# Kernel optimization log

Measured on AMD Instinct MI355X. Metric: run time of the kernel, lower is better.

Reference implementation:

```python
import jax, jax.numpy as jnp
import numpy as np

B, N, DIM = 2, 2048, 1024
NUM_HEADS = 16
EFF = NUM_HEADS // 2          # 8 effective heads
HD = DIM // NUM_HEADS         # 64
LAMBDA_INIT = 0.8
EPS = 1e-5


def setup_inputs() -> dict:
    key = jax.random.key(0)
    ks = jax.random.split(key, 16)
    s = 0.02
    return {
        "x":  jax.random.normal(ks[0], (B, N, DIM), dtype=jnp.float32),
        "Wq": jax.random.normal(ks[1], (DIM, DIM), dtype=jnp.float32) * s,
        "bq": jnp.zeros((DIM,), dtype=jnp.float32),
        "Wk": jax.random.normal(ks[2], (DIM, DIM), dtype=jnp.float32) * s,
        "bk": jnp.zeros((DIM,), dtype=jnp.float32),
        "Wv": jax.random.normal(ks[3], (DIM, DIM), dtype=jnp.float32) * s,
        "bv": jnp.zeros((DIM,), dtype=jnp.float32),
        "Wo": jax.random.normal(ks[4], (DIM, DIM), dtype=jnp.float32) * s,
        "bo": jnp.zeros((DIM,), dtype=jnp.float32),
        "norm_w": jnp.ones((2 * HD,), dtype=jnp.float32),
        "lq1": jax.random.normal(ks[5], (HD,), dtype=jnp.float32) * 0.1,
        "lk1": jax.random.normal(ks[6], (HD,), dtype=jnp.float32) * 0.1,
        "lq2": jax.random.normal(ks[7], (HD,), dtype=jnp.float32) * 0.1,
        "lk2": jax.random.normal(ks[8], (HD,), dtype=jnp.float32) * 0.1,
    }


def reference(x, Wq, bq, Wk, bk, Wv, bv, Wo, bo, norm_w, lq1, lk1, lq2, lk2):
    scale = HD ** -0.5
    # projections (torch Linear: y = x @ W.T + b)
    q = (x @ Wq.T + bq).reshape(B, N, NUM_HEADS, HD).transpose(0, 2, 1, 3) * scale  # [B,2E,N,hd]
    k = (x @ Wk.T + bk).reshape(B, N, NUM_HEADS, HD).transpose(0, 2, 1, 3)          # [B,2E,N,hd]
    v = (x @ Wv.T + bv).reshape(B, N, EFF, 2 * HD).transpose(0, 2, 1, 3)            # [B,E,N,2hd]

    scores = jnp.einsum('bhqd,bhkd->bhqk', q, k)              # [B,2E,N,N]
    probs = jax.nn.softmax(scores, axis=-1)
    probs = probs.reshape(B, EFF, 2, N, N)                    # pair consecutive heads

    lam = jnp.exp(jnp.sum(lq1 * lk1)) - jnp.exp(jnp.sum(lq2 * lk2)) + LAMBDA_INIT
    diff = probs[:, :, 0] - lam * probs[:, :, 1]              # [B,E,N,N]

    out = jnp.einsum('behk,bekd->behd'.replace('e','h').replace('hh','h') if False else 'bhqk,bhkd->bhqd', diff, v)  # [B,E,N,2hd]
    # headwise RMSNorm over last dim (2*hd)
    out = out * jax.lax.rsqrt(jnp.mean(out * out, axis=-1, keepdims=True) + EPS) * norm_w
    out = out * (1.0 - LAMBDA_INIT)

    out = out.transpose(0, 2, 1, 3).reshape(B, N, DIM)
    return out @ Wo.T + bo
```

## Files before the change

kernel.cpp:

```cpp
#include <hip/hip_runtime.h>
#include <hip/hip_bf16.h>

#define B_   2
#define N_   2048
#define DIM_ 1024
#define HD_  64
#define DV_  128

typedef __bf16 bf16;
typedef __bf16 bf16x8 __attribute__((ext_vector_type(8)));
typedef __bf16 bf16x4 __attribute__((ext_vector_type(4)));
typedef float  floatx4 __attribute__((ext_vector_type(4)));
typedef float  floatx16 __attribute__((ext_vector_type(16)));
typedef unsigned int uint;
typedef uint uint2v __attribute__((ext_vector_type(2)));
typedef uint uint4v __attribute__((ext_vector_type(4)));

#if __has_builtin(__builtin_amdgcn_exp2f)
#define EXP2(x) __builtin_amdgcn_exp2f(x)
#else
#define EXP2(x) exp2f(x)
#endif

#define QSCALE 0.1803368801111244f

__device__ __forceinline__ void async16(const void* g, void* l) {
  __builtin_amdgcn_global_load_lds(
      (__attribute__((address_space(1))) void*)g,
      (__attribute__((address_space(3))) void*)l, 16, 0, 0);
}

__device__ __forceinline__ uint packbf(float a, float b) {
  unsigned short ul = __builtin_bit_cast(unsigned short, (bf16)a);
  unsigned short uh = __builtin_bit_cast(unsigned short, (bf16)b);
  return (uint)ul | ((uint)uh << 16);
}

__global__ void convert_kernel(const float* __restrict__ x,
                               const float* __restrict__ wq,
                               const float* __restrict__ wk,
                               const float* __restrict__ wv,
                               const float* __restrict__ wo,
                               bf16* __restrict__ dst) {
  const int NX = B_ * N_ * DIM_;
  const int NW = DIM_ * DIM_;
  int i = (blockIdx.x * 256 + threadIdx.x) * 4;
  const float* src;
  int off;
  if (i < NX) { src = x; off = i; }
  else {
    int j = i - NX;
    int w = j >> 20;
    off = j & (NW - 1);
    src = (w == 0) ? wq : (w == 1) ? wk : (w == 2) ? wv : wo;
  }
  float4 v = *(const float4*)(src + off);
  bf16x4 o = { (bf16)v.x, (bf16)v.y, (bf16)v.z, (bf16)v.w };
  *(bf16x4*)(dst + i) = o;
}

__global__ void lam_kernel(const float* __restrict__ lq1, const float* __restrict__ lk1,
                           const float* __restrict__ lq2, const float* __restrict__ lk2,
                           float* __restrict__ lam_out) {
  int l = threadIdx.x;
  float a = lq1[l] * lk1[l];
  float b = lq2[l] * lk2[l];
  for (int m = 1; m < 64; m <<= 1) {
    a += __shfl_xor(a, m, 64);
    b += __shfl_xor(b, m, 64);
  }
  if (l == 0) *lam_out = __expf(a) - __expf(b) + 0.8f;
}

__global__ __launch_bounds__(256) void proj_kernel(
    const bf16* __restrict__ xb, const bf16* __restrict__ wall,
    const float* __restrict__ bq, const float* __restrict__ bk,
    const float* __restrict__ bv,
    bf16* __restrict__ qo, bf16* __restrict__ ko, bf16* __restrict__ vt) {
  __shared__ __align__(16) bf16 SM[2 * 128 * 64];
  bf16* At = SM;
  bf16* Bt = SM + 128 * 64;
  const int tid = threadIdx.x, lane = tid & 63, w = tid >> 6;
  const int tm = blockIdx.x, tn = blockIdx.y, z = blockIdx.z;
  const int quad = lane >> 4, l15 = lane & 15;
  const int wm = (w >> 1) * 64, wn = (w & 1) * 64;
  const bf16* Ab = xb + (long)tm * 128 * DIM_;
  const bf16* Bb = wall + (long)z * (DIM_ * DIM_) + (long)tn * 128 * DIM_;
  floatx4 zero = {0.f, 0.f, 0.f, 0.f};
  floatx4 acc[4][4];
#pragma unroll
  for (int i = 0; i < 4; ++i)
#pragma unroll
    for (int j = 0; j < 4; ++j) acc[i][j] = zero;

  for (int kb = 0; kb < DIM_ / 64; ++kb) {
    for (int idx = tid; idx < 1024; idx += 256) {
      int row = idx >> 3, ch = idx & 7, g = ch ^ (row & 7);
      async16(Ab + row * DIM_ + kb * 64 + g * 8, (char*)At + (idx - lane) * 16);
      async16(Bb + row * DIM_ + kb * 64 + g * 8, (char*)Bt + (idx - lane) * 16);
    }
    __syncthreads();
#pragma unroll
    for (int ks = 0; ks < 2; ++ks) {
      bf16x8 af[4], bfm[4];
#pragma unroll
      for (int mt = 0; mt < 4; ++mt) {
        int r = wm + mt * 16 + l15;
        af[mt] = *(const bf16x8*)&At[r * 64 + ((ks * 4 + quad) ^ (r & 7)) * 8];
      }
#pragma unroll
      for (int nt = 0; nt < 4; ++nt) {
        int r = wn + nt * 16 + l15;
        bfm[nt] = *(const bf16x8*)&Bt[r * 64 + ((ks * 4 + quad) ^ (r & 7)) * 8];
      }
#pragma unroll
      for (int mt = 0; mt < 4; ++mt)
#pragma unroll
        for (int nt = 0; nt < 4; ++nt)
          acc[mt][nt] = __builtin_amdgcn_mfma_f32_16x16x32_bf16(
              af[mt], bfm[nt], acc[mt][nt], 0, 0, 0);
    }
    __syncthreads();
  }

  if (z != 2) {
#pragma unroll
    for (int mt = 0; mt < 4; ++mt)
#pragma unroll
      for (int nt = 0; nt < 4; ++nt)
#pragma unroll
        for (int r = 0; r < 4; ++r) {
          int grow = tm * 128 + wm + mt * 16 + quad * 4 + r;
          int gcol = tn * 128 + wn + nt * 16 + l15;
          float v = acc[mt][nt][r];
          if (z == 0) {
            qo[(long)grow * DIM_ + gcol] = (bf16)((v + bq[gcol]) * QSCALE);
          } else {
            ko[(long)grow * DIM_ + gcol] = (bf16)(v + bk[gcol]);
          }
        }
  } else {
    bf16* Vl = SM;
#pragma unroll
    for (int nt = 0; nt < 4; ++nt) {
      int d = wn + nt * 16 + l15;
      float bvv = bv[tn * 128 + d];
      int m = (d & 7) * 2;
#pragma unroll
      for (int mt = 0; mt < 4; ++mt) {
        bf16x4 v4 = { (bf16)(acc[mt][nt][0] + bvv), (bf16)(acc[mt][nt][1] + bvv),
                      (bf16)(acc[mt][nt][2] + bvv), (bf16)(acc[mt][nt][3] + bvv) };
        int c = (wm >> 2) + mt * 4 + quad;
        *(bf16x4*)&Vl[d * 128 + (c ^ m) * 4] = v4;
      }
    }
    __syncthreads();
    const int bb = tm >> 4, e = tn;
    const long rowbase = ((long)(bb * 8 + e) * 128) * (long)N_ + (tm & 15) * 128;
#pragma unroll
    for (int p = 0; p < 8; ++p) {
      int d = p * 16 + (tid >> 4), j = tid & 15;
      int cs = (2 * j) ^ ((d & 7) * 2);
      bf16x8 val = *(const bf16x8*)&Vl[d * 128 + cs * 4];
      *(bf16x8*)&vt[rowbase + (long)d * N_ + j * 8] = val;
    }
  }
}

__global__ __launch_bounds__(256, 1) void attn_kernel(
    const bf16* __restrict__ qb, const bf16* __restrict__ kbuf,
    const bf16* __restrict__ vt, const float* __restrict__ lamp,
    const float* __restrict__ norm_w, bf16* __restrict__ ao) {
  __shared__ __align__(16) char smem[65536];

  const int tid = threadIdx.x, lane = tid & 63, w = tid >> 6;
  const int qt = blockIdx.x, e = blockIdx.y, b = blockIdx.z;
  const int hl = w & 1, qh = w >> 1;
  const int h = lane >> 5, l31 = lane & 31;
  const int qbase = qt * 128 + qh * 64;

  bf16x8 qf[2][4];
#pragma unroll
  for (int qs = 0; qs < 2; ++qs) {
    const bf16* qrp = qb + (long)(b * N_ + qbase + qs * 32 + l31) * DIM_
                      + e * 128 + hl * 64 + h * 8;
#pragma unroll
    for (int c = 0; c < 4; ++c) qf[qs][c] = *(const bf16x8*)(qrp + c * 16);
  }

  const bf16* kbase = kbuf + (long)b * N_ * DIM_ + e * 128;
  const bf16* vbase = vt + (long)(b * 8 + e) * DV_ * N_;

  floatx16 acc[2][4];
#pragma unroll
  for (int qs = 0; qs < 2; ++qs)
#pragma unroll
    for (int dt = 0; dt < 4; ++dt) acc[qs][dt] = floatx16{};
  float lp[2] = {0.f, 0.f};

#define STAGE(ktv, bufv)                                                            \
  {                                                                                 \
    int kt_ = (ktv);                                                                \
    char* kdst = smem + (bufv) * 16384;                                             \
    char* vdst = smem + 32768 + (bufv) * 16384;                                     \
    _Pragma("unroll") for (int t = 0; t < 4; ++t) {                                 \
      int idx = tid + t * 256;                                                      \
      int khl = idx >> 9, row = (idx >> 3) & 63, ch = idx & 7;                      \
      int g = ch ^ (row & 7) ^ ((row >> 3) & 3);                                    \
      async16(kbase + ((long)(kt_ * 64 + row)) * DIM_ + khl * 64 + g * 8,           \
              kdst + (idx - lane) * 16);                                            \
    }                                                                               \
    _Pragma("unroll") for (int t = 0; t < 4; ++t) {                                 \
      int idx = tid + t * 256;                                                      \
      int row = idx >> 3, ch = idx & 7;                                             \
      int g = ch ^ (row & 7) ^ ((row >> 3) & 3);                                    \
      async16(vbase + (long)row * N_ + kt_ * 64 + g * 8,                            \
              vdst + (idx - lane) * 16);                                            \
    }                                                                               \
  }

  STAGE(0, 0);

  for (int kt = 0; kt < N_ / 64; ++kt) {
    const int buf = kt & 1;
    __syncthreads();
    if (kt + 1 < N_ / 64) STAGE(kt + 1, buf ^ 1);

    const bf16* Kh = (const bf16*)(smem + buf * 16384) + hl * 4096;
    const bf16* Vb = (const bf16*)(smem + 32768 + buf * 16384);

    bf16x8 kfrag[2][4], vfrag[4][4];
#pragma unroll
    for (int kt2 = 0; kt2 < 2; ++kt2)
#pragma unroll
      for (int c = 0; c < 4; ++c) {
        int row = kt2 * 32 + l31;
        int sw = (c * 2 + h) ^ (row & 7) ^ ((row >> 3) & 3);
        kfrag[kt2][c] = *(const bf16x8*)&Kh[row * 64 + sw * 8];
      }
#pragma unroll
    for (int dt = 0; dt < 4; ++dt)
#pragma unroll
      for (int kc = 0; kc < 4; ++kc) {
        int row = dt * 32 + l31;
        int sw = (kc * 2 + h) ^ (row & 7) ^ ((row >> 3) & 3);
        vfrag[dt][kc] = *(const bf16x8*)&Vb[row * 64 + sw * 8];
      }

#pragma unroll
    for (int qs = 0; qs < 2; ++qs) {
      bf16x8 af[2][2];
#pragma unroll
      for (int kt2 = 0; kt2 < 2; ++kt2) {
        floatx16 sv{};
#pragma unroll
        for (int c = 0; c < 4; ++c)
          sv = __builtin_amdgcn_mfma_f32_32x32x16_bf16(kfrag[kt2][c], qf[qs][c], sv, 0, 0, 0);
        float t[16];
        float s = 0.f;
#pragma unroll
        for (int i = 0; i < 16; ++i) { t[i] = EXP2(sv[i]); s += t[i]; }
        lp[qs] += s;
        uint d0 = packbf(t[0], t[1]),   d1 = packbf(t[2], t[3]);
        uint d2 = packbf(t[4], t[5]),   d3 = packbf(t[6], t[7]);
        uint d4 = packbf(t[8], t[9]),   d5 = packbf(t[10], t[11]);
        uint d6 = packbf(t[12], t[13]), d7 = packbf(t[14], t[15]);
        uint4v f0, f1;
#if __has_builtin(__builtin_amdgcn_permlane32_swap)
        uint2v r02 = __builtin_amdgcn_permlane32_swap(d0, d2, false, false);
        uint2v r13 = __builtin_amdgcn_permlane32_swap(d1, d3, false, false);
        f0 = uint4v{r02.x, r13.x, r02.y, r13.y};
        uint2v r46 = __builtin_amdgcn_permlane32_swap(d4, d6, false, false);
        uint2v r57 = __builtin_amdgcn_permlane32_swap(d5, d7, false, false);
        f1 = uint4v{r46.x, r57.x, r46.y, r57.y};
#else
        uint e0 = __shfl_xor((int)d0, 32, 64), e1 = __shfl_xor((int)d1, 32, 64);
        uint e2 = __shfl_xor((int)d2, 32, 64), e3 = __shfl_xor((int)d3, 32, 64);
        uint e4 = __shfl_xor((int)d4, 32, 64), e5 = __shfl_xor((int)d5, 32, 64);
        uint e6 = __shfl_xor((int)d6, 32, 64), e7 = __shfl_xor((int)d7, 32, 64);
        f0 = h ? uint4v{e2, e3, d2, d3} : uint4v{d0, d1, e0, e1};
        f1 = h ? uint4v{e6, e7, d6, d7} : uint4v{d4, d5, e4, e5};
#endif
        af[kt2][0] = __builtin_bit_cast(bf16x8, f0);
        af[kt2][1] = __builtin_bit_cast(bf16x8, f1);
      }
#pragma unroll
      for (int dt = 0; dt < 4; ++dt)
#pragma unroll
        for (int kt2 = 0; kt2 < 2; ++kt2)
#pragma unroll
          for (int u = 0; u < 2; ++u)
            acc[qs][dt] = __builtin_amdgcn_mfma_f32_32x32x16_bf16(
                af[kt2][u], vfrag[dt][kt2 * 2 + u], acc[qs][dt], 0, 0, 0);
    }
  }

  lp[0] += __shfl_xor(lp[0], 32, 64);
  lp[1] += __shfl_xor(lp[1], 32, 64);

  float* Ob = (float*)smem;
  __syncthreads();

  if (hl == 1) {
#pragma unroll
    for (int qs = 0; qs < 2; ++qs)
#pragma unroll
      for (int r = 0; r < 16; ++r) {
        int qloc = (r & 3) + 8 * (r >> 2) + 4 * h;
        float inv = 1.0f / __shfl(lp[qs], qloc, 64);
        float* row = &Ob[(qh * 64 + qs * 32 + qloc) * 128 + l31];
#pragma unroll
        for (int dt = 0; dt < 4; ++dt) row[dt * 32] = acc[qs][dt][r] * inv;
      }
  }
  __syncthreads();
  if (hl == 0) {
    float lam = *lamp;
    float nw4[4];
#pragma unroll
    for (int dt = 0; dt < 4; ++dt) nw4[dt] = norm_w[dt * 32 + l31] * 0.2f;
#pragma unroll
    for (int qs = 0; qs < 2; ++qs)
#pragma unroll
      for (int r = 0; r < 16; ++r) {
        int qloc = (r & 3) + 8 * (r >> 2) + 4 * h;
        float inv = 1.0f / __shfl(lp[qs], qloc, 64);
        const float* row = &Ob[(qh * 64 + qs * 32 + qloc) * 128 + l31];
        float v[4], ss = 0.f;
#pragma unroll
        for (int dt = 0; dt < 4; ++dt) {
          v[dt] = acc[qs][dt][r] * inv - lam * row[dt * 32];
          ss += v[dt] * v[dt];
        }
#pragma unroll
        for (int msk = 1; msk < 32; msk <<= 1) ss += __shfl_xor(ss, msk, 64);
        float rms = rsqrtf(ss * (1.0f / 128.0f) + 1e-5f);
        int n = qbase + qs * 32 + qloc;
        bf16* dst = ao + (long)(b * N_ + n) * DIM_ + e * DV_ + l31;
#pragma unroll
        for (int dt = 0; dt < 4; ++dt) dst[dt * 32] = (bf16)(v[dt] * rms * nw4[dt]);
      }
  }
}

__global__ __launch_bounds__(512) void out_gemm(
    const bf16* __restrict__ ab, const bf16* __restrict__ wo,
    const float* __restrict__ bo, float* __restrict__ out) {
  __shared__ __align__(16) bf16 At[128 * 64];
  __shared__ __align__(16) bf16 Bt[128 * 64];
  const int tid = threadIdx.x, lane = tid & 63, w = tid >> 6;
  const int tm = blockIdx.x, tn = blockIdx.y;
  const int quad = lane >> 4, l15 = lane & 15;
  const int wm = (w & 3) * 32, wn = (w >> 2) * 64;
  const bf16* Ab = ab + (long)tm * 128 * DIM_;
  const bf16* Bb = wo + (long)tn * 128 * DIM_;
  floatx4 zero = {0.f, 0.f, 0.f, 0.f};
  floatx4 acc[2][4];
#pragma unroll
  for (int i = 0; i < 2; ++i)
#pragma unroll
    for (int j = 0; j < 4; ++j) acc[i][j] = zero;

  for (int kb = 0; kb < DIM_ / 64; ++kb) {
    for (int idx = tid; idx < 1024; idx += 512) {
      int row = idx >> 3, ch = idx & 7, g = ch ^ (row & 7);
      async16(Ab + row * DIM_ + kb * 64 + g * 8, (char*)At + (idx - lane) * 16);
      async16(Bb + row * DIM_ + kb * 64 + g * 8, (char*)Bt + (idx - lane) * 16);
    }
    __syncthreads();
#pragma unroll
    for (int ks = 0; ks < 2; ++ks) {
      bf16x8 af[2], bfm[4];
#pragma unroll
      for (int mt = 0; mt < 2; ++mt) {
        int r = wm + mt * 16 + l15;
        af[mt] = *(const bf16x8*)&At[r * 64 + ((ks * 4 + quad) ^ (r & 7)) * 8];
      }
#pragma unroll
      for (int nt = 0; nt < 4; ++nt) {
        int r = wn + nt * 16 + l15;
        bfm[nt] = *(const bf16x8*)&Bt[r * 64 + ((ks * 4 + quad) ^ (r & 7)) * 8];
      }
#pragma unroll
      for (int mt = 0; mt < 2; ++mt)
#pragma unroll
        for (int nt = 0; nt < 4; ++nt)
          acc[mt][nt] = __builtin_amdgcn_mfma_f32_16x16x32_bf16(
              af[mt], bfm[nt], acc[mt][nt], 0, 0, 0);
    }
    __syncthreads();
  }
#pragma unroll
  for (int mt = 0; mt < 2; ++mt)
#pragma unroll
    for (int nt = 0; nt < 4; ++nt)
#pragma unroll
      for (int r = 0; r < 4; ++r) {
        int grow = tm * 128 + wm + mt * 16 + quad * 4 + r;
        int gcol = tn * 128 + wn + nt * 16 + l15;
        out[(long)grow * DIM_ + gcol] = acc[mt][nt][r] + bo[gcol];
      }
}

extern "C" void kernel_launch(void* const* d_in, const int* in_sizes, int n_in,
                              void* d_out, int out_size, void* d_ws, size_t ws_size,
                              hipStream_t stream) {
  const float* x    = (const float*)d_in[0];
  const float* Wq   = (const float*)d_in[1];
  const float* bq   = (const float*)d_in[2];
  const float* Wk   = (const float*)d_in[3];
  const float* bk   = (const float*)d_in[4];
  const float* Wv   = (const float*)d_in[5];
  const float* bv   = (const float*)d_in[6];
  const float* Wo   = (const float*)d_in[7];
  const float* bo   = (const float*)d_in[8];
  const float* nw   = (const float*)d_in[9];
  const float* lq1  = (const float*)d_in[10];
  const float* lk1  = (const float*)d_in[11];
  const float* lq2  = (const float*)d_in[12];
  const float* lk2  = (const float*)d_in[13];

  char* ws = (char*)d_ws;
  float* lam = (float*)ws;
  bf16* xb   = (bf16*)(ws + 256);
  bf16* wqb  = xb + 4194304;
  bf16* qb   = wqb + 4 * 1048576;
  bf16* kbuf = qb + 4194304;
  bf16* vtb  = kbuf + 4194304;
  bf16* ab   = vtb + 4194304;

  convert_kernel<<<8192, 256, 0, stream>>>(x, Wq, Wk, Wv, Wo, xb);
  lam_kernel<<<1, 64, 0, stream>>>(lq1, lk1, lq2, lk2, lam);
  proj_kernel<<<dim3(32, 8, 3), 256, 0, stream>>>(xb, wqb, bq, bk, bv, qb, kbuf, vtb);
  attn_kernel<<<dim3(16, 8, 2), 256, 0, stream>>>(qb, kbuf, vtb, lam, nw, ab);
  out_gemm<<<dim3(32, 8), 512, 0, stream>>>(ab, wqb + 3 * 1048576, bo, (float*)d_out);
}
```

Before: 222.5 us.

## Split attention work across 8 waves with one 32-row query slice each

```diff
diff --git a/kernel.cpp b/kernel.cpp
--- a/kernel.cpp
+++ b/kernel.cpp
@@ -167,7 +167,7 @@
   }
 }
 
-__global__ __launch_bounds__(256, 1) void attn_kernel(
+__global__ __launch_bounds__(512, 2) void attn_kernel(
     const bf16* __restrict__ qb, const bf16* __restrict__ kbuf,
     const bf16* __restrict__ vt, const float* __restrict__ lamp,
     const float* __restrict__ norm_w, bf16* __restrict__ ao) {
@@ -177,41 +177,38 @@
   const int qt = blockIdx.x, e = blockIdx.y, b = blockIdx.z;
   const int hl = w & 1, qh = w >> 1;
   const int h = lane >> 5, l31 = lane & 31;
-  const int qbase = qt * 128 + qh * 64;
-
-  bf16x8 qf[2][4];
-#pragma unroll
-  for (int qs = 0; qs < 2; ++qs) {
-    const bf16* qrp = qb + (long)(b * N_ + qbase + qs * 32 + l31) * DIM_
+  const int qbase = qt * 128;
+
+  bf16x8 qf[4];
+  {
+    const bf16* qrp = qb + (long)(b * N_ + qbase + qh * 32 + l31) * DIM_
                       + e * 128 + hl * 64 + h * 8;
 #pragma unroll
-    for (int c = 0; c < 4; ++c) qf[qs][c] = *(const bf16x8*)(qrp + c * 16);
+    for (int c = 0; c < 4; ++c) qf[c] = *(const bf16x8*)(qrp + c * 16);
   }
 
   const bf16* kbase = kbuf + (long)b * N_ * DIM_ + e * 128;
   const bf16* vbase = vt + (long)(b * 8 + e) * DV_ * N_;
 
-  floatx16 acc[2][4];
-#pragma unroll
-  for (int qs = 0; qs < 2; ++qs)
-#pragma unroll
-    for (int dt = 0; dt < 4; ++dt) acc[qs][dt] = floatx16{};
-  float lp[2] = {0.f, 0.f};
+  floatx16 acc[4];
+#pragma unroll
+  for (int dt = 0; dt < 4; ++dt) acc[dt] = floatx16{};
+  float lp = 0.f;
 
 #define STAGE(ktv, bufv)                                                            \
   {                                                                                 \
     int kt_ = (ktv);                                                                \
     char* kdst = smem + (bufv) * 16384;                                             \
     char* vdst = smem + 32768 + (bufv) * 16384;                                     \
-    _Pragma("unroll") for (int t = 0; t < 4; ++t) {                                 \
-      int idx = tid + t * 256;                                                      \
+    _Pragma("unroll") for (int t = 0; t < 2; ++t) {                                 \
+      int idx = tid + t * 512;                                                      \
       int khl = idx >> 9, row = (idx >> 3) & 63, ch = idx & 7;                      \
       int g = ch ^ (row & 7) ^ ((row >> 3) & 3);                                    \
       async16(kbase + ((long)(kt_ * 64 + row)) * DIM_ + khl * 64 + g * 8,           \
               kdst + (idx - lane) * 16);                                            \
     }                                                                               \
-    _Pragma("unroll") for (int t = 0; t < 4; ++t) {                                 \
-      int idx = tid + t * 256;                                                      \
+    _Pragma("unroll") for (int t = 0; t < 2; ++t) {                                 \
+      int idx = tid + t * 512;                                                      \
       int row = idx >> 3, ch = idx & 7;                                             \
       int g = ch ^ (row & 7) ^ ((row >> 3) & 3);                                    \
       async16(vbase + (long)row * N_ + kt_ * 64 + g * 8,                            \
@@ -247,71 +244,65 @@
         vfrag[dt][kc] = *(const bf16x8*)&Vb[row * 64 + sw * 8];
       }
 
-#pragma unroll
-    for (int qs = 0; qs < 2; ++qs) {
-      bf16x8 af[2][2];
-#pragma unroll
-      for (int kt2 = 0; kt2 < 2; ++kt2) {
-        floatx16 sv{};
-#pragma unroll
-        for (int c = 0; c < 4; ++c)
-          sv = __builtin_amdgcn_mfma_f32_32x32x16_bf16(kfrag[kt2][c], qf[qs][c], sv, 0, 0, 0);
-        float t[16];
-        float s = 0.f;
-#pragma unroll
-        for (int i = 0; i < 16; ++i) { t[i] = EXP2(sv[i]); s += t[i]; }
-        lp[qs] += s;
-        uint d0 = packbf(t[0], t[1]),   d1 = packbf(t[2], t[3]);
-        uint d2 = packbf(t[4], t[5]),   d3 = packbf(t[6], t[7]);
-        uint d4 = packbf(t[8], t[9]),   d5 = packbf(t[10], t[11]);
-        uint d6 = packbf(t[12], t[13]), d7 = packbf(t[14], t[15]);
-        uint4v f0, f1;
+    bf16x8 af[2][2];
+#pragma unroll
+    for (int kt2 = 0; kt2 < 2; ++kt2) {
+      floatx16 sv{};
+#pragma unroll
+      for (int c = 0; c < 4; ++c)
+        sv = __builtin_amdgcn_mfma_f32_32x32x16_bf16(kfrag[kt2][c], qf[c], sv, 0, 0, 0);
+      float t[16];
+      float s = 0.f;
+#pragma unroll
+      for (int i = 0; i < 16; ++i) { t[i] = EXP2(sv[i]); s += t[i]; }
+      lp += s;
+      uint d0 = packbf(t[0], t[1]),   d1 = packbf(t[2], t[3]);
+      uint d2 = packbf(t[4], t[5]),   d3 = packbf(t[6], t[7]);
+      uint d4 = packbf(t[8], t[9]),   d5 = packbf(t[10], t[11]);
+      uint d6 = packbf(t[12], t[13]), d7 = packbf(t[14], t[15]);
+      uint4v f0, f1;
 #if __has_builtin(__builtin_amdgcn_permlane32_swap)
-        uint2v r02 = __builtin_amdgcn_permlane32_swap(d0, d2, false, false);
-        uint2v r13 = __builtin_amdgcn_permlane32_swap(d1, d3, false, false);
-        f0 = uint4v{r02.x, r13.x, r02.y, r13.y};
-        uint2v r46 = __builtin_amdgcn_permlane32_swap(d4, d6, false, false);
-        uint2v r57 = __builtin_amdgcn_permlane32_swap(d5, d7, false, false);
-        f1 = uint4v{r46.x, r57.x, r46.y, r57.y};
+      uint2v r02 = __builtin_amdgcn_permlane32_swap(d0, d2, false, false);
+      uint2v r13 = __builtin_amdgcn_permlane32_swap(d1, d3, false, false);
+      f0 = uint4v{r02.x, r13.x, r02.y, r13.y};
+      uint2v r46 = __builtin_amdgcn_permlane32_swap(d4, d6, false, false);
+      uint2v r57 = __builtin_amdgcn_permlane32_swap(d5, d7, false, false);
+      f1 = uint4v{r46.x, r57.x, r46.y, r57.y};
 #else
-        uint e0 = __shfl_xor((int)d0, 32, 64), e1 = __shfl_xor((int)d1, 32, 64);
-        uint e2 = __shfl_xor((int)d2, 32, 64), e3 = __shfl_xor((int)d3, 32, 64);
-        uint e4 = __shfl_xor((int)d4, 32, 64), e5 = __shfl_xor((int)d5, 32, 64);
-        uint e6 = __shfl_xor((int)d6, 32, 64), e7 = __shfl_xor((int)d7, 32, 64);
-        f0 = h ? uint4v{e2, e3, d2, d3} : uint4v{d0, d1, e0, e1};
-        f1 = h ? uint4v{e6, e7, d6, d7} : uint4v{d4, d5, e4, e5};
+      uint e0 = __shfl_xor((int)d0, 32, 64), e1 = __shfl_xor((int)d1, 32, 64);
+      uint e2 = __shfl_xor((int)d2, 32, 64), e3 = __shfl_xor((int)d3, 32, 64);
+      uint e4 = __shfl_xor((int)d4, 32, 64), e5 = __shfl_xor((int)d5, 32, 64);
+      uint e6 = __shfl_xor((int)d6, 32, 64), e7 = __shfl_xor((int)d7, 32, 64);
+      f0 = h ? uint4v{e2, e3, d2, d3} : uint4v{d0, d1, e0, e1};
+      f1 = h ? uint4v{e6, e7, d6, d7} : uint4v{d4, d5, e4, e5};
 #endif
-        af[kt2][0] = __builtin_bit_cast(bf16x8, f0);
-        af[kt2][1] = __builtin_bit_cast(bf16x8, f1);
-      }
-#pragma unroll
-      for (int dt = 0; dt < 4; ++dt)
-#pragma unroll
-        for (int kt2 = 0; kt2 < 2; ++kt2)
-#pragma unroll
-          for (int u = 0; u < 2; ++u)
-            acc[qs][dt] = __builtin_amdgcn_mfma_f32_32x32x16_bf16(
-                af[kt2][u], vfrag[dt][kt2 * 2 + u], acc[qs][dt], 0, 0, 0);
-    }
-  }
-
-  lp[0] += __shfl_xor(lp[0], 32, 64);
-  lp[1] += __shfl_xor(lp[1], 32, 64);
+      af[kt2][0] = __builtin_bit_cast(bf16x8, f0);
+      af[kt2][1] = __builtin_bit_cast(bf16x8, f1);
+    }
+#pragma unroll
+    for (int dt = 0; dt < 4; ++dt)
+#pragma unroll
+      for (int kt2 = 0; kt2 < 2; ++kt2)
+#pragma unroll
+        for (int u = 0; u < 2; ++u)
+          acc[dt] = __builtin_amdgcn_mfma_f32_32x32x16_bf16(
+              af[kt2][u], vfrag[dt][kt2 * 2 + u], acc[dt], 0, 0, 0);
+  }
+
+  lp += __shfl_xor(lp, 32, 64);
 
   float* Ob = (float*)smem;
   __syncthreads();
 
   if (hl == 1) {
 #pragma unroll
-    for (int qs = 0; qs < 2; ++qs)
-#pragma unroll
-      for (int r = 0; r < 16; ++r) {
-        int qloc = (r & 3) + 8 * (r >> 2) + 4 * h;
-        float inv = 1.0f / __shfl(lp[qs], qloc, 64);
-        float* row = &Ob[(qh * 64 + qs * 32 + qloc) * 128 + l31];
-#pragma unroll
-        for (int dt = 0; dt < 4; ++dt) row[dt * 32] = acc[qs][dt][r] * inv;
-      }
+    for (int r = 0; r < 16; ++r) {
+      int qloc = (r & 3) + 8 * (r >> 2) + 4 * h;
+      float inv = 1.0f / __shfl(lp, qloc, 64);
+      float* row = &Ob[(qh * 32 + qloc) * 128 + l31];
+#pragma unroll
+      for (int dt = 0; dt < 4; ++dt) row[dt * 32] = acc[dt][r] * inv;
+    }
   }
   __syncthreads();
   if (hl == 0) {
@@ -320,26 +311,24 @@
 #pragma unroll
     for (int dt = 0; dt < 4; ++dt) nw4[dt] = norm_w[dt * 32 + l31] * 0.2f;
 #pragma unroll
-    for (int qs = 0; qs < 2; ++qs)
-#pragma unroll
-      for (int r = 0; r < 16; ++r) {
-        int qloc = (r & 3) + 8 * (r >> 2) + 4 * h;
-        float inv = 1.0f / __shfl(lp[qs], qloc, 64);
-        const float* row = &Ob[(qh * 64 + qs * 32 + qloc) * 128 + l31];
-        float v[4], ss = 0.f;
-#pragma unroll
-        for (int dt = 0; dt < 4; ++dt) {
-          v[dt] = acc[qs][dt][r] * inv - lam * row[dt * 32];
-          ss += v[dt] * v[dt];
-        }
-#pragma unroll
-        for (int msk = 1; msk < 32; msk <<= 1) ss += __shfl_xor(ss, msk, 64);
-        float rms = rsqrtf(ss * (1.0f / 128.0f) + 1e-5f);
-        int n = qbase + qs * 32 + qloc;
-        bf16* dst = ao + (long)(b * N_ + n) * DIM_ + e * DV_ + l31;
-#pragma unroll
-        for (int dt = 0; dt < 4; ++dt) dst[dt * 32] = (bf16)(v[dt] * rms * nw4[dt]);
-      }
+    for (int r = 0; r < 16; ++r) {
+      int qloc = (r & 3) + 8 * (r >> 2) + 4 * h;
+      float inv = 1.0f / __shfl(lp, qloc, 64);
+      const float* row = &Ob[(qh * 32 + qloc) * 128 + l31];
+      float v[4], ss = 0.f;
+#pragma unroll
+      for (int dt = 0; dt < 4; ++dt) {
+        v[dt] = acc[dt][r] * inv - lam * row[dt * 32];
+        ss += v[dt] * v[dt];
+      }
+#pragma unroll
+      for (int msk = 1; msk < 32; msk <<= 1) ss += __shfl_xor(ss, msk, 64);
+      float rms = rsqrtf(ss * (1.0f / 128.0f) + 1e-5f);
+      int n = qbase + qh * 32 + qloc;
+      bf16* dst = ao + (long)(b * N_ + n) * DIM_ + e * DV_ + l31;
+#pragma unroll
+      for (int dt = 0; dt < 4; ++dt) dst[dt * 32] = (bf16)(v[dt] * rms * nw4[dt]);
+    }
   }
 }
 
@@ -432,6 +421,6 @@
   convert_kernel<<<8192, 256, 0, stream>>>(x, Wq, Wk, Wv, Wo, xb);
   lam_kernel<<<1, 64, 0, stream>>>(lq1, lk1, lq2, lk2, lam);
   proj_kernel<<<dim3(32, 8, 3), 256, 0, stream>>>(xb, wqb, bq, bk, bv, qb, kbuf, vtb);
-  attn_kernel<<<dim3(16, 8, 2), 256, 0, stream>>>(qb, kbuf, vtb, lam, nw, ab);
+  attn_kernel<<<dim3(16, 8, 2), 512, 0, stream>>>(qb, kbuf, vtb, lam, nw, ab);
   out_gemm<<<dim3(32, 8), 512, 0, stream>>>(ab, wqb + 3 * 1048576, bo, (float*)d_out);
 }
```

Measured after the change: 212.5 us. 4.5% less time.
